# Kernel optimization log

Measured on AMD Instinct MI355X. Metric: run time of the kernel, lower is better.

## Reference

```python
import jax, jax.numpy as jnp
import numpy as np

EPS = 1e-06  # slot-attention renorm epsilon
LN_EPS = 1e-05  # torch LayerNorm default
NUM_ITERS = 3


def layernorm(x, w, b):
    m = jnp.mean(x, axis=-1, keepdims=True)
    v = jnp.mean((x - m) ** 2, axis=-1, keepdims=True)
    return (x - m) * jax.lax.rsqrt(v + LN_EPS) * w + b


def setup_inputs() -> dict:
    key = jax.random.key(0)
    ks = jax.random.split(key, 16)
    B, N, D = 32, 4096, 512
    S, NS, H = 128, 8, 256
    def lin(k, out_f, in_f):
        return jax.random.normal(k, (out_f, in_f), jnp.float32) * (1.0 / np.sqrt(in_f))
    return {
        "inputs": jax.random.normal(ks[0], (B, N, D), jnp.float32),
        "slots_init": jax.random.normal(ks[1], (B, NS, S), jnp.float32),
        "ln_in_w": jnp.ones((D,), jnp.float32), "ln_in_b": jnp.zeros((D,), jnp.float32),
        "ln_slot_w": jnp.ones((S,), jnp.float32), "ln_slot_b": jnp.zeros((S,), jnp.float32),
        "ln_mlp_w": jnp.ones((S,), jnp.float32), "ln_mlp_b": jnp.zeros((S,), jnp.float32),
        "Wq": lin(ks[2], S, S), "Wk": lin(ks[3], S, D), "Wv": lin(ks[4], S, D),
        "gru_Wih": lin(ks[5], 3 * S, S), "gru_Whh": lin(ks[6], 3 * S, S),
        "gru_bih": jnp.zeros((3 * S,), jnp.float32), "gru_bhh": jnp.zeros((3 * S,), jnp.float32),
        "mlp_W1": lin(ks[7], H, S), "mlp_b1": jnp.zeros((H,), jnp.float32),
        "mlp_W2": lin(ks[8], S, H), "mlp_b2": jnp.zeros((S,), jnp.float32),
        "slots_mu": jax.random.normal(ks[9], (1, 1, S), jnp.float32) * 0.1,
        "slots_log_sigma": jax.random.normal(ks[10], (1, 1, S), jnp.float32) * 0.1,
    }


def gru_cell(x, h, Wih, Whh, bih, bhh):
    # PyTorch GRUCell math. x, h: [BS, S]
    S = h.shape[-1]
    gi = x @ Wih.T + bih
    gh = h @ Whh.T + bhh
    i_r, i_z, i_n = gi[:, :S], gi[:, S:2 * S], gi[:, 2 * S:]
    h_r, h_z, h_n = gh[:, :S], gh[:, S:2 * S], gh[:, 2 * S:]
    r = jax.nn.sigmoid(i_r + h_r)
    z = jax.nn.sigmoid(i_z + h_z)
    n = jnp.tanh(i_n + r * h_n)
    return (1.0 - z) * n + z * h


def reference(inputs, slots_init, ln_in_w, ln_in_b, ln_slot_w, ln_slot_b, ln_mlp_w, ln_mlp_b,
              Wq, Wk, Wv, gru_Wih, gru_Whh, gru_bih, gru_bhh,
              mlp_W1, mlp_b1, mlp_W2, mlp_b2, slots_mu, slots_log_sigma):
    B, N, D = inputs.shape
    NS, S = slots_init.shape[1], slots_init.shape[2]
    x = layernorm(inputs, ln_in_w, ln_in_b)
    k = jnp.einsum('bnd,sd->bns', x, Wk)  # [B,N,S]
    v = jnp.einsum('bnd,sd->bns', x, Wv)
    slots = slots_mu + jnp.exp(slots_log_sigma) * slots_init  # [B,NS,S]
    scale = S ** (-0.5)
    for _ in range(NUM_ITERS):
        slots_prev = slots
        q = jnp.einsum('bmd,sd->bms', layernorm(slots, ln_slot_w, ln_slot_b), Wq)  # [B,NS,S]
        attn_logits = scale * jnp.einsum('bns,bms->bnm', k, q)  # [B,N,NS]
        attn = jax.nn.softmax(attn_logits, axis=-1) + EPS
        attn = attn / jnp.sum(attn, axis=1, keepdims=True)  # normalize over inputs
        updates = jnp.einsum('bnm,bns->bms', attn, v)  # [B,NS,S]
        h = gru_cell(updates.reshape(B * NS, S), slots_prev.reshape(B * NS, S),
                     gru_Wih, gru_Whh, gru_bih, gru_bhh).reshape(B, NS, S)
        mlp_out = jnp.maximum(layernorm(h, ln_mlp_w, ln_mlp_b) @ mlp_W1.T + mlp_b1, 0.0) @ mlp_W2.T + mlp_b2
        slots = h + mlp_out
    return slots
```

## Files before the change

### kernel.cpp

```cpp
#include <hip/hip_runtime.h>

typedef __bf16 v8bf __attribute__((ext_vector_type(8)));
typedef __bf16 v4bf __attribute__((ext_vector_type(4)));
typedef float  v4f  __attribute__((ext_vector_type(4)));
typedef unsigned short u16;

#define LN_EPS_F 1e-5f
#define ATTN_EPS 1e-6f

static constexpr int Bsz = 32;
static constexpr int Nn  = 4096;
static constexpr int Dd  = 512;
static constexpr int Ss  = 128;
static constexpr int NSs = 8;
static constexpr int Hh  = 256;
static constexpr int MROWS = Bsz * Nn;

__device__ __forceinline__ void load_lds16(const void* g, void* l) {
    __builtin_amdgcn_global_load_lds(
        (const __attribute__((address_space(1))) void*)g,
        (__attribute__((address_space(3))) void*)l, 16, 0, 0);
}

__global__ __launch_bounds__(256) void k_prep(const float* __restrict__ Wk, const float* __restrict__ Wv,
                                              const float* __restrict__ ln_in_w, const float* __restrict__ ln_in_b,
                                              const float* __restrict__ slots_init, const float* __restrict__ mu,
                                              const float* __restrict__ lsig,
                                              u16* __restrict__ Wkvp, float* __restrict__ cb,
                                              float* __restrict__ Scol, float* __restrict__ slots) {
    const int bid = blockIdx.x;
    const int t = threadIdx.x;
    if (bid < 512) {
        int idx = bid * 256 + t;
        int n = idx >> 9, d = idx & 511;
        float w = (n < Ss) ? Wk[n * Dd + d] : Wv[(n - Ss) * Dd + d];
        w *= ln_in_w[d];
        __bf16 bv = (__bf16)w;
        Wkvp[idx] = __builtin_bit_cast(u16, bv);
    } else if (bid < 640) {
        int idx = (bid - 512) * 256 + t;
        int sidx = idx & (Ss - 1);
        slots[idx] = mu[sidx] + expf(lsig[sidx]) * slots_init[idx];
    } else {
        const int wid = t >> 6, lane = t & 63;
        const int rowbase = (bid - 640) * 32 + wid * 8;
        const int d0 = lane * 8;
        float4 lw0 = *reinterpret_cast<const float4*>(ln_in_w + d0);
        float4 lw1 = *reinterpret_cast<const float4*>(ln_in_w + d0 + 4);
        float4 lb0 = *reinterpret_cast<const float4*>(ln_in_b + d0);
        float4 lb1 = *reinterpret_cast<const float4*>(ln_in_b + d0 + 4);
        for (int rr = 0; rr < 8; ++rr) {
            int row = rowbase + rr;
            const float* wrow = (row < Ss) ? (Wk + (size_t)row * Dd)
                                           : (Wv + (size_t)(row - Ss) * Dd);
            float4 w0 = *reinterpret_cast<const float4*>(wrow + d0);
            float4 w1 = *reinterpret_cast<const float4*>(wrow + d0 + 4);
            float accb = lb0.x*w0.x + lb0.y*w0.y + lb0.z*w0.z + lb0.w*w0.w
                       + lb1.x*w1.x + lb1.y*w1.y + lb1.z*w1.z + lb1.w*w1.w;
            float accs = (float)(__bf16)(w0.x*lw0.x) + (float)(__bf16)(w0.y*lw0.y)
                       + (float)(__bf16)(w0.z*lw0.z) + (float)(__bf16)(w0.w*lw0.w)
                       + (float)(__bf16)(w1.x*lw1.x) + (float)(__bf16)(w1.y*lw1.y)
                       + (float)(__bf16)(w1.z*lw1.z) + (float)(__bf16)(w1.w*lw1.w);
#pragma unroll
            for (int off = 32; off > 0; off >>= 1) {
                accb += __shfl_xor(accb, off);
                accs += __shfl_xor(accs, off);
            }
            if (lane == 0) { cb[row] = accb; Scol[row] = accs; }
        }
    }
}

__global__ __launch_bounds__(256) void k_kvgemm(const float* __restrict__ X,
                                                const u16* __restrict__ Wkvp,
                                                const float* __restrict__ cb,
                                                const float* __restrict__ Scol,
                                                u16* __restrict__ kv) {
    __shared__ __bf16 As[64][72];
    __shared__ __bf16 Bs[2][256 * 64];
    __shared__ float2 stats_sh[64];
    const int t    = threadIdx.x;
    const int lane = t & 63;
    const int wid  = t >> 6;
    const size_t m0 = (size_t)blockIdx.x * 64;

    const int ar  = t >> 2;
    const int ac0 = (t & 3) * 16;
    const float* xrow = X + (m0 + ar) * Dd;

    const int sub  = lane >> 3;
    const int scol = ((lane & 7) ^ sub) * 8;
    const u16* bsrc = Wkvp + (size_t)(wid * 64 + sub) * Dd + scol;

    const v4f vzero = {0.f, 0.f, 0.f, 0.f};
    v4f acc[4][4];
#pragma unroll
    for (int i = 0; i < 4; ++i)
#pragma unroll
        for (int j = 0; j < 4; ++j) acc[i][j] = vzero;

    const int g  = lane >> 4;
    const int lr = lane & 15;
    float s1 = 0.f, s2 = 0.f;

    float4 a_pre[4];
#pragma unroll
    for (int j = 0; j < 4; ++j)
        a_pre[j] = *reinterpret_cast<const float4*>(xrow + ac0 + j * 4);
#pragma unroll
    for (int p = 0; p < 8; ++p)
        load_lds16(bsrc + (size_t)p * 8 * Dd, &Bs[0][(wid * 64 + p * 8) * 64]);
#pragma unroll
    for (int p = 0; p < 8; ++p)
        load_lds16(bsrc + (size_t)p * 8 * Dd + 64, &Bs[1][(wid * 64 + p * 8) * 64]);

#pragma unroll
    for (int kb = 0; kb < 8; ++kb) {
#pragma unroll
        for (int j = 0; j < 4; ++j) {
            float4 xv = a_pre[j];
            s1 += xv.x + xv.y + xv.z + xv.w;
            s2 += xv.x * xv.x + xv.y * xv.y + xv.z * xv.z + xv.w * xv.w;
            v4bf wv;
            wv[0] = (__bf16)xv.x; wv[1] = (__bf16)xv.y;
            wv[2] = (__bf16)xv.z; wv[3] = (__bf16)xv.w;
            *reinterpret_cast<v4bf*>(&As[ar][ac0 + j * 4]) = wv;
        }
        if (kb < 7) {
#pragma unroll
            for (int j = 0; j < 4; ++j)
                a_pre[j] = *reinterpret_cast<const float4*>(xrow + (kb + 1) * 64 + ac0 + j * 4);
        }
        if (kb < 7)
            asm volatile("s_waitcnt vmcnt(12) lgkmcnt(0)\ns_barrier" ::: "memory");
        else
            asm volatile("s_waitcnt vmcnt(0) lgkmcnt(0)\ns_barrier" ::: "memory");
        {
            const __bf16* bbase = &Bs[kb & 1][0];
#pragma unroll
            for (int ks = 0; ks < 2; ++ks) {
                v8bf a[4], bfr[4];
#pragma unroll
                for (int mi = 0; mi < 4; ++mi)
                    a[mi] = *reinterpret_cast<const v8bf*>(&As[mi * 16 + lr][ks * 32 + g * 8]);
#pragma unroll
                for (int ni = 0; ni < 4; ++ni) {
                    int r = wid * 64 + ni * 16 + lr;
                    bfr[ni] = *reinterpret_cast<const v8bf*>(
                        &bbase[r * 64 + ((ks * 32 + g * 8) ^ ((lr & 7) * 8))]);
                }
#pragma unroll
                for (int mi = 0; mi < 4; ++mi)
#pragma unroll
                    for (int ni = 0; ni < 4; ++ni)
                        acc[mi][ni] = __builtin_amdgcn_mfma_f32_16x16x32_bf16(a[mi], bfr[ni], acc[mi][ni], 0, 0, 0);
            }
        }
        asm volatile("s_barrier" ::: "memory");
        if (kb < 6) {
#pragma unroll
            for (int p = 0; p < 8; ++p)
                load_lds16(bsrc + (size_t)p * 8 * Dd + (kb + 2) * 64,
                           &Bs[kb & 1][(wid * 64 + p * 8) * 64]);
        }
    }
    s1 += __shfl_xor(s1, 1); s1 += __shfl_xor(s1, 2);
    s2 += __shfl_xor(s2, 1); s2 += __shfl_xor(s2, 2);
    if ((t & 3) == 0) {
        float m = s1 * (1.f / Dd);
        float v = s2 * (1.f / Dd) - m * m;
        stats_sh[ar] = make_float2(m, rsqrtf(v + LN_EPS_F));
    }
    __syncthreads();
    float Sn[4], cbv[4];
#pragma unroll
    for (int ni = 0; ni < 4; ++ni) {
        int ng = wid * 64 + ni * 16 + lr;
        Sn[ni]  = Scol[ng];
        cbv[ni] = cb[ng];
    }
#pragma unroll
    for (int mi = 0; mi < 4; ++mi)
#pragma unroll
        for (int j = 0; j < 4; ++j) {
            float2 st = stats_sh[mi * 16 + g * 4 + j];
            size_t mg = m0 + mi * 16 + g * 4 + j;
#pragma unroll
            for (int ni = 0; ni < 4; ++ni) {
                int ng = wid * 64 + ni * 16 + lr;
                float val = st.y * (acc[mi][ni][j] - st.x * Sn[ni]) + cbv[ni];
                __bf16 bv = (__bf16)val;
                kv[mg * 256 + ng] = __builtin_bit_cast(u16, bv);
            }
        }
}

__global__ __launch_bounds__(128) void k_q(const float* __restrict__ slots,
                                           const float* __restrict__ lnw, const float* __restrict__ lnb,
                                           const float* __restrict__ Wq, float* __restrict__ q) {
    __shared__ float xs[128];
    __shared__ float red[4];
    const int t = threadIdx.x;
    const int bm = blockIdx.x;
    float x = slots[bm * 128 + t];
    float s = x, s2 = x * x;
#pragma unroll
    for (int off = 32; off > 0; off >>= 1) { s += __shfl_xor(s, off); s2 += __shfl_xor(s2, off); }
    const int wid = t >> 6, lane = t & 63;
    if (lane == 0) { red[wid * 2] = s; red[wid * 2 + 1] = s2; }
    __syncthreads();
    float S1 = red[0] + red[2], S2 = red[1] + red[3];
    float m = S1 * (1.f / 128.f);
    float rstd = rsqrtf(S2 * (1.f / 128.f) - m * m + LN_EPS_F);
    xs[t] = (x - m) * rstd * lnw[t] + lnb[t];
    __syncthreads();
    const float* wr = Wq + (size_t)t * 128;
    float acc = 0.f;
#pragma unroll 8
    for (int d = 0; d < 128; d += 4) {
        float4 w = *reinterpret_cast<const float4*>(wr + d);
        acc += w.x * xs[d] + w.y * xs[d + 1] + w.z * xs[d + 2] + w.w * xs[d + 3];
    }
    q[bm * 128 + t] = acc * 0.08838834764831845f;
}

__global__ __launch_bounds__(256) void k_attnupd(const u16* __restrict__ kv, const float* __restrict__ q,
                                                 float* __restrict__ upd_part, float* __restrict__ colsum_part) {
    __shared__ float qs[8 * 128];
    __shared__ float at[128][8];
    __shared__ __bf16 vt[128][128];
    __shared__ float colpart[4][8];
    const int b  = blockIdx.y;
    const int ch = blockIdx.x;
    const int t  = threadIdx.x;
    const int lane = t & 63, wv = t >> 6;
    *reinterpret_cast<float4*>(&qs[t * 4]) = *reinterpret_cast<const float4*>(&q[b * 1024 + t * 4]);
    __syncthreads();
    {
        const int rsub = lane >> 4;
        const int csub = (lane & 15) * 8;
#pragma unroll
        for (int p = 0; p < 8; ++p) {
            int row = wv * 32 + p * 4;
            const u16* src = kv + ((size_t)(b * Nn + ch * 128 + row + rsub)) * 256 + 128 + csub;
            load_lds16(src, &vt[row][0]);
        }
    }
    const int nl   = t >> 1;
    const int half = t & 1;
    const u16* krow = kv + ((size_t)(b * Nn + ch * 128 + nl)) * 256 + half * 64;
    float acc[8] = {0.f, 0.f, 0.f, 0.f, 0.f, 0.f, 0.f, 0.f};
#pragma unroll
    for (int c = 0; c < 8; ++c) {
        v8bf kvv = *reinterpret_cast<const v8bf*>(krow + c * 8);
        float kf[8];
#pragma unroll
        for (int j = 0; j < 8; ++j) kf[j] = (float)kvv[j];
#pragma unroll
        for (int m = 0; m < 8; ++m) {
            const float* qrow = &qs[m * 128 + half * 64 + c * 8];
            float aa = 0.f;
#pragma unroll
            for (int j = 0; j < 8; ++j) aa += kf[j] * qrow[j];
            acc[m] += aa;
        }
    }
#pragma unroll
    for (int m = 0; m < 8; ++m) acc[m] += __shfl_xor(acc[m], 1);
    float mx = acc[0];
#pragma unroll
    for (int m = 1; m < 8; ++m) mx = fmaxf(mx, acc[m]);
    float e[8]; float ssum = 0.f;
#pragma unroll
    for (int m = 0; m < 8; ++m) { e[m] = __expf(acc[m] - mx); ssum += e[m]; }
    float inv = 1.0f / ssum;
    float a8[8];
#pragma unroll
    for (int m = 0; m < 8; ++m) a8[m] = e[m] * inv + ATTN_EPS;
    *reinterpret_cast<float4*>(&at[nl][half * 4]) =
        make_float4(a8[half * 4], a8[half * 4 + 1], a8[half * 4 + 2], a8[half * 4 + 3]);
#pragma unroll
    for (int m = 0; m < 8; ++m) {
        float v = a8[m];
#pragma unroll
        for (int off = 32; off > 0; off >>= 1) v += __shfl_xor(v, off);
        if (lane == 0) colpart[wv][m] = v * 0.5f;
    }
    __syncthreads();
    const int m2 = t >> 5;
    const int s0 = (t & 31) * 4;
    float a0 = 0.f, a1 = 0.f, a2 = 0.f, a3 = 0.f;
#pragma unroll 4
    for (int n = 0; n < 128; ++n) {
        float a = at[n][m2];
        v4bf vvv = *reinterpret_cast<const v4bf*>(&vt[n][s0]);
        a0 += a * (float)vvv[0];
        a1 += a * (float)vvv[1];
        a2 += a * (float)vvv[2];
        a3 += a * (float)vvv[3];
    }
    *reinterpret_cast<float4*>(upd_part + ((size_t)(b * 32 + ch) * 8 + m2) * 128 + s0) =
        make_float4(a0, a1, a2, a3);
    if (t < 8)
        colsum_part[(b * 32 + ch) * 8 + t] =
            colpart[0][t] + colpart[1][t] + colpart[2][t] + colpart[3][t];
}

__global__ __launch_bounds__(256) void k_finishq(const float* __restrict__ upd_part,
                                                 const float* __restrict__ colsum_part,
                                                 const float* __restrict__ slots_in,
                                                 const float* __restrict__ Wih, const float* __restrict__ Whh,
                                                 const float* __restrict__ bih, const float* __restrict__ bhh,
                                                 const float* __restrict__ lnw, const float* __restrict__ lnb,
                                                 const float* __restrict__ W1, const float* __restrict__ b1,
                                                 const float* __restrict__ W2, const float* __restrict__ b2,
                                                 const float* __restrict__ lnsw, const float* __restrict__ lnsb,
                                                 const float* __restrict__ Wq,
                                                 float* __restrict__ slots_out, float* __restrict__ qout) {
    __shared__ float us[128], sp[128], hnorm[128], qsrc[128], act[256];
    __shared__ float upart[2][128];
    __shared__ float gpart[2][6][128];
    __shared__ float p2[2][128];
    __shared__ float qpart[2][128];
    __shared__ float red[4];
    __shared__ float csum_sh;
    const int t   = threadIdx.x;
    const int tid = t & 127, half = t >> 7;
    const int bm  = blockIdx.x;
    const int b = bm >> 3, m = bm & 7;
    if (t < 64) {
        float v = (t < 32) ? colsum_part[(b * 32 + t) * 8 + m] : 0.f;
#pragma unroll
        for (int off = 32; off > 0; off >>= 1) v += __shfl_xor(v, off);
        if (t == 0) csum_sh = v;
    }
    float u = 0.f;
#pragma unroll 4
    for (int chk = half * 16; chk < half * 16 + 16; ++chk)
        u += upd_part[((size_t)(b * 32 + chk) * 8 + m) * 128 + tid];
    upart[half][tid] = u;
    if (half == 0) sp[tid] = slots_in[bm * 128 + tid];
    __syncthreads();
    if (half == 0) us[tid] = (upart[0][tid] + upart[1][tid]) * (1.f / csum_sh);
    __syncthreads();
    {
        const int d0g = half * 64;
        float a_r = 0.f, a_z = 0.f, a_n = 0.f, b_r = 0.f, b_z = 0.f, b_n = 0.f;
        const float* Wr = Wih + (size_t)tid * 128 + d0g;
        const float* Wz = Wih + (size_t)(128 + tid) * 128 + d0g;
        const float* Wn = Wih + (size_t)(256 + tid) * 128 + d0g;
        const float* Vr = Whh + (size_t)tid * 128 + d0g;
        const float* Vz = Whh + (size_t)(128 + tid) * 128 + d0g;
        const float* Vn = Whh + (size_t)(256 + tid) * 128 + d0g;
#pragma unroll 4
        for (int d = 0; d < 64; d += 4) {
            float u0 = us[d0g + d], u1 = us[d0g + d + 1], u2 = us[d0g + d + 2], u3 = us[d0g + d + 3];
            float p0 = sp[d0g + d], p1 = sp[d0g + d + 1], p2_ = sp[d0g + d + 2], p3 = sp[d0g + d + 3];
            float4 w;
            w = *reinterpret_cast<const float4*>(Wr + d); a_r += w.x*u0 + w.y*u1 + w.z*u2 + w.w*u3;
            w = *reinterpret_cast<const float4*>(Wz + d); a_z += w.x*u0 + w.y*u1 + w.z*u2 + w.w*u3;
            w = *reinterpret_cast<const float4*>(Wn + d); a_n += w.x*u0 + w.y*u1 + w.z*u2 + w.w*u3;
            w = *reinterpret_cast<const float4*>(Vr + d); b_r += w.x*p0 + w.y*p1 + w.z*p2_ + w.w*p3;
            w = *reinterpret_cast<const float4*>(Vz + d); b_z += w.x*p0 + w.y*p1 + w.z*p2_ + w.w*p3;
            w = *reinterpret_cast<const float4*>(Vn + d); b_n += w.x*p0 + w.y*p1 + w.z*p2_ + w.w*p3;
        }
        gpart[half][0][tid] = a_r; gpart[half][1][tid] = a_z; gpart[half][2][tid] = a_n;
        gpart[half][3][tid] = b_r; gpart[half][4][tid] = b_z; gpart[half][5][tid] = b_n;
    }
    __syncthreads();
    float gir = bih[tid]       + gpart[0][0][tid] + gpart[1][0][tid];
    float giz = bih[128 + tid] + gpart[0][1][tid] + gpart[1][1][tid];
    float gin = bih[256 + tid] + gpart[0][2][tid] + gpart[1][2][tid];
    float ghr = bhh[tid]       + gpart[0][3][tid] + gpart[1][3][tid];
    float ghz = bhh[128 + tid] + gpart[0][4][tid] + gpart[1][4][tid];
    float ghn = bhh[256 + tid] + gpart[0][5][tid] + gpart[1][5][tid];
    float h0 = sp[tid];
    float r  = 1.f / (1.f + __expf(-(gir + ghr)));
    float z  = 1.f / (1.f + __expf(-(giz + ghz)));
    float nn = tanhf(gin + r * ghn);
    float h  = (1.f - z) * nn + z * h0;
    if (half == 0) {
        float s = h, s2 = h * h;
#pragma unroll
        for (int off = 32; off > 0; off >>= 1) { s += __shfl_xor(s, off); s2 += __shfl_xor(s2, off); }
        if ((t & 63) == 0) { red[(tid >> 6) * 2] = s; red[(tid >> 6) * 2 + 1] = s2; }
    }
    __syncthreads();
    {
        float S1 = red[0] + red[2], S2 = red[1] + red[3];
        float mean = S1 * (1.f / Ss);
        float rstd = rsqrtf(S2 * (1.f / Ss) - mean * mean + LN_EPS_F);
        if (half == 0) hnorm[tid] = (h - mean) * rstd * lnw[tid] + lnb[tid];
    }
    __syncthreads();
    {
        float a = b1[t];
        const float* w1r = W1 + (size_t)t * 128;
#pragma unroll 4
        for (int d = 0; d < 128; d += 4) {
            float4 w = *reinterpret_cast<const float4*>(w1r + d);
            a += w.x * hnorm[d] + w.y * hnorm[d + 1] + w.z * hnorm[d + 2] + w.w * hnorm[d + 3];
        }
        act[t] = fmaxf(a, 0.f);
    }
    __syncthreads();
    {
        float o = 0.f;
        const int j0 = half * 128;
        const float* w2r = W2 + (size_t)tid * 256 + j0;
#pragma unroll 4
        for (int j = 0; j < 128; j += 4) {
            float4 w = *reinterpret_cast<const float4*>(w2r + j);
            o += w.x * act[j0 + j] + w.y * act[j0 + j + 1] + w.z * act[j0 + j + 2] + w.w * act[j0 + j + 3];
        }
        p2[half][tid] = o;
    }
    __syncthreads();
    float snew = h + b2[tid] + p2[0][tid] + p2[1][tid];
    if (half == 0) slots_out[bm * 128 + tid] = snew;
    if (half == 0) {
        float s = snew, s2 = snew * snew;
#pragma unroll
        for (int off = 32; off > 0; off >>= 1) { s += __shfl_xor(s, off); s2 += __shfl_xor(s2, off); }
        if ((t & 63) == 0) { red[(tid >> 6) * 2] = s; red[(tid >> 6) * 2 + 1] = s2; }
    }
    __syncthreads();
    {
        float T1 = red[0] + red[2], T2 = red[1] + red[3];
        float m2 = T1 * (1.f / Ss);
        float rstd2 = rsqrtf(T2 * (1.f / Ss) - m2 * m2 + LN_EPS_F);
        if (half == 0) qsrc[tid] = (snew - m2) * rstd2 * lnsw[tid] + lnsb[tid];
    }
    __syncthreads();
    {
        float qa = 0.f;
        const int d0g = half * 64;
        const float* wr = Wq + (size_t)tid * 128 + d0g;
#pragma unroll 4
        for (int d = 0; d < 64; d += 4) {
            float4 w = *reinterpret_cast<const float4*>(wr + d);
            qa += w.x * qsrc[d0g + d] + w.y * qsrc[d0g + d + 1] + w.z * qsrc[d0g + d + 2] + w.w * qsrc[d0g + d + 3];
        }
        qpart[half][tid] = qa;
    }
    __syncthreads();
    if (half == 0)
        qout[bm * 128 + tid] = (qpart[0][tid] + qpart[1][tid]) * 0.08838834764831845f;
}

extern "C" void kernel_launch(void* const* d_in, const int* in_sizes, int n_in,
                              void* d_out, int out_size, void* d_ws, size_t ws_size,
                              hipStream_t stream) {
    const float* X          = (const float*)d_in[0];
    const float* slots_init = (const float*)d_in[1];
    const float* ln_in_w    = (const float*)d_in[2];
    const float* ln_in_b    = (const float*)d_in[3];
    const float* ln_slot_w  = (const float*)d_in[4];
    const float* ln_slot_b  = (const float*)d_in[5];
    const float* ln_mlp_w   = (const float*)d_in[6];
    const float* ln_mlp_b   = (const float*)d_in[7];
    const float* Wq         = (const float*)d_in[8];
    const float* Wk         = (const float*)d_in[9];
    const float* Wv         = (const float*)d_in[10];
    const float* gWih       = (const float*)d_in[11];
    const float* gWhh       = (const float*)d_in[12];
    const float* gbih       = (const float*)d_in[13];
    const float* gbhh       = (const float*)d_in[14];
    const float* W1         = (const float*)d_in[15];
    const float* b1         = (const float*)d_in[16];
    const float* W2         = (const float*)d_in[17];
    const float* b2         = (const float*)d_in[18];
    const float* mu         = (const float*)d_in[19];
    const float* lsig       = (const float*)d_in[20];

    char* p = (char*)d_ws;
    u16*    Wkvp        = (u16*)p;    p += (size_t)256 * 512 * sizeof(u16);
    float*  cb          = (float*)p;  p += 256 * sizeof(float);
    float*  Scol        = (float*)p;  p += 256 * sizeof(float);
    float*  slots       = (float*)p;  p += 32 * 8 * 128 * sizeof(float);
    float*  qbuf        = (float*)p;  p += 32 * 8 * 128 * sizeof(float);
    float*  colsum_part = (float*)p;  p += 32 * 32 * 8 * sizeof(float);
    float*  upd_part    = (float*)p;  p += (size_t)32 * 32 * 8 * 128 * sizeof(float);
    u16*    kv          = (u16*)p;    p += (size_t)MROWS * 256 * sizeof(u16);

    k_prep<<<648, 256, 0, stream>>>(Wk, Wv, ln_in_w, ln_in_b, slots_init, mu, lsig,
                                    Wkvp, cb, Scol, slots);
    k_kvgemm<<<MROWS / 64, 256, 0, stream>>>(X, Wkvp, cb, Scol, kv);
    k_q<<<256, 128, 0, stream>>>(slots, ln_slot_w, ln_slot_b, Wq, qbuf);

    for (int it = 0; it < 3; ++it) {
        k_attnupd<<<dim3(32, 32), 256, 0, stream>>>(kv, qbuf, upd_part, colsum_part);
        k_finishq<<<256, 256, 0, stream>>>(upd_part, colsum_part, slots,
                                           gWih, gWhh, gbih, gbhh,
                                           ln_mlp_w, ln_mlp_b, W1, b1, W2, b2,
                                           ln_slot_w, ln_slot_b, Wq,
                                           (it == 2) ? (float*)d_out : slots, qbuf);
    }
}
```

Before: 306.6 us.

## Load K/V weight fragments directly to registers and stage output through LDS

The fused LayerNorm+KV GEMM kernel no longer double-buffers the weight tile in LDS via global_load_lds. Each wave now loads its B fragments straight from global memory (L2-resident) into registers, prefetching the next k-block while the MFMAs run. The freed LDS holds an output staging buffer so the bf16 results are written with coalesced 16-byte stores instead of scattered 2-byte stores. Launch bounds request 3 blocks per CU to raise occupancy. The cost is extra register pressure and possibly uncoalesced global B reads per lane.

Result: slower. 455.3 us (+48.5%).

```diff
diff --git a/kernel.cpp b/kernel.cpp
--- a/kernel.cpp
+++ b/kernel.cpp
@@ -71,13 +71,13 @@
     }
 }
 
-__global__ __launch_bounds__(256) void k_kvgemm(const float* __restrict__ X,
-                                                const u16* __restrict__ Wkvp,
-                                                const float* __restrict__ cb,
-                                                const float* __restrict__ Scol,
-                                                u16* __restrict__ kv) {
+__global__ __launch_bounds__(256, 3) void k_kvgemm(const float* __restrict__ X,
+                                                   const u16* __restrict__ Wkvp,
+                                                   const float* __restrict__ cb,
+                                                   const float* __restrict__ Scol,
+                                                   u16* __restrict__ kv) {
     __shared__ __bf16 As[64][72];
-    __shared__ __bf16 Bs[2][256 * 64];
+    __shared__ u16 outbuf[64][264];
     __shared__ float2 stats_sh[64];
     const int t    = threadIdx.x;
     const int lane = t & 63;
@@ -88,9 +88,9 @@
     const int ac0 = (t & 3) * 16;
     const float* xrow = X + (m0 + ar) * Dd;
 
-    const int sub  = lane >> 3;
-    const int scol = ((lane & 7) ^ sub) * 8;
-    const u16* bsrc = Wkvp + (size_t)(wid * 64 + sub) * Dd + scol;
+    const int g  = lane >> 4;
+    const int lr = lane & 15;
+    const u16* bptr = Wkvp + (size_t)(wid * 64 + lr) * Dd + g * 8;
 
     const v4f vzero = {0.f, 0.f, 0.f, 0.f};
     v4f acc[4][4];
@@ -99,20 +99,18 @@
 #pragma unroll
         for (int j = 0; j < 4; ++j) acc[i][j] = vzero;
 
-    const int g  = lane >> 4;
-    const int lr = lane & 15;
     float s1 = 0.f, s2 = 0.f;
 
     float4 a_pre[4];
 #pragma unroll
     for (int j = 0; j < 4; ++j)
         a_pre[j] = *reinterpret_cast<const float4*>(xrow + ac0 + j * 4);
-#pragma unroll
-    for (int p = 0; p < 8; ++p)
-        load_lds16(bsrc + (size_t)p * 8 * Dd, &Bs[0][(wid * 64 + p * 8) * 64]);
-#pragma unroll
-    for (int p = 0; p < 8; ++p)
-        load_lds16(bsrc + (size_t)p * 8 * Dd + 64, &Bs[1][(wid * 64 + p * 8) * 64]);
+    v8bf bfr[8];
+#pragma unroll
+    for (int ks = 0; ks < 2; ++ks)
+#pragma unroll
+        for (int ni = 0; ni < 4; ++ni)
+            bfr[ks * 4 + ni] = *reinterpret_cast<const v8bf*>(bptr + (size_t)ni * 16 * Dd + ks * 32);
 
 #pragma unroll
     for (int kb = 0; kb < 8; ++kb) {
@@ -131,38 +129,25 @@
             for (int j = 0; j < 4; ++j)
                 a_pre[j] = *reinterpret_cast<const float4*>(xrow + (kb + 1) * 64 + ac0 + j * 4);
         }
-        if (kb < 7)
-            asm volatile("s_waitcnt vmcnt(12) lgkmcnt(0)\ns_barrier" ::: "memory");
-        else
-            asm volatile("s_waitcnt vmcnt(0) lgkmcnt(0)\ns_barrier" ::: "memory");
-        {
-            const __bf16* bbase = &Bs[kb & 1][0];
-#pragma unroll
-            for (int ks = 0; ks < 2; ++ks) {
-                v8bf a[4], bfr[4];
+        __syncthreads();
+#pragma unroll
+        for (int ks = 0; ks < 2; ++ks) {
+            v8bf a[4];
+#pragma unroll
+            for (int mi = 0; mi < 4; ++mi)
+                a[mi] = *reinterpret_cast<const v8bf*>(&As[mi * 16 + lr][ks * 32 + g * 8]);
+#pragma unroll
+            for (int ni = 0; ni < 4; ++ni) {
+                v8bf bcur = bfr[ks * 4 + ni];
 #pragma unroll
                 for (int mi = 0; mi < 4; ++mi)
-                    a[mi] = *reinterpret_cast<const v8bf*>(&As[mi * 16 + lr][ks * 32 + g * 8]);
-#pragma unroll
-                for (int ni = 0; ni < 4; ++ni) {
-                    int r = wid * 64 + ni * 16 + lr;
-                    bfr[ni] = *reinterpret_cast<const v8bf*>(
-                        &bbase[r * 64 + ((ks * 32 + g * 8) ^ ((lr & 7) * 8))]);
-                }
-#pragma unroll
-                for (int mi = 0; mi < 4; ++mi)
-#pragma unroll
-                    for (int ni = 0; ni < 4; ++ni)
-                        acc[mi][ni] = __builtin_amdgcn_mfma_f32_16x16x32_bf16(a[mi], bfr[ni], acc[mi][ni], 0, 0, 0);
+                    acc[mi][ni] = __builtin_amdgcn_mfma_f32_16x16x32_bf16(a[mi], bcur, acc[mi][ni], 0, 0, 0);
+                if (kb < 7)
+                    bfr[ks * 4 + ni] = *reinterpret_cast<const v8bf*>(
+                        bptr + (size_t)ni * 16 * Dd + (kb + 1) * 64 + ks * 32);
             }
         }
-        asm volatile("s_barrier" ::: "memory");
-        if (kb < 6) {
-#pragma unroll
-            for (int p = 0; p < 8; ++p)
-                load_lds16(bsrc + (size_t)p * 8 * Dd + (kb + 2) * 64,
-                           &Bs[kb & 1][(wid * 64 + p * 8) * 64]);
-        }
+        __syncthreads();
     }
     s1 += __shfl_xor(s1, 1); s1 += __shfl_xor(s1, 2);
     s2 += __shfl_xor(s2, 1); s2 += __shfl_xor(s2, 2);
@@ -184,15 +169,23 @@
 #pragma unroll
         for (int j = 0; j < 4; ++j) {
             float2 st = stats_sh[mi * 16 + g * 4 + j];
-            size_t mg = m0 + mi * 16 + g * 4 + j;
 #pragma unroll
             for (int ni = 0; ni < 4; ++ni) {
-                int ng = wid * 64 + ni * 16 + lr;
                 float val = st.y * (acc[mi][ni][j] - st.x * Sn[ni]) + cbv[ni];
                 __bf16 bv = (__bf16)val;
-                kv[mg * 256 + ng] = __builtin_bit_cast(u16, bv);
+                outbuf[mi * 16 + g * 4 + j][wid * 64 + ni * 16 + lr] = __builtin_bit_cast(u16, bv);
             }
         }
+    __syncthreads();
+    {
+        const int orow = t >> 2;
+        const int ocol = (t & 3) * 64;
+        u16* dst = kv + (m0 + orow) * 256 + ocol;
+        const u16* src = &outbuf[orow][ocol];
+#pragma unroll
+        for (int c = 0; c < 8; ++c)
+            *reinterpret_cast<uint4*>(dst + c * 8) = *reinterpret_cast<const uint4*>(src + c * 8);
+    }
 }
 
 __global__ __launch_bounds__(128) void k_q(const float* __restrict__ slots,
```
